# Optimization experiments

Measured on AMD Instinct MI355X. Metric: run time of the kernel, lower is better.

## Reference

```python
import jax, jax.numpy as jnp
import numpy as np

NT, NRV, NR = 100000, 200000, 300000  # tile / road_vertex / road node counts
E = 400000                             # edges per edge type
B, H, P, A = 64, 128, 64, 512          # graphs, hidden, player_state_dim, action_dim


def _gat(h_src, h_dst, src, dst, W, a_s, a_d, b, n_dst):
    # PyG GATConv, heads=1, shared lin for src/dst, no self loops (bipartite)
    hs = h_src @ W                      # [Ns, H]
    hd = h_dst @ W                      # [Nd, H]
    e = jax.nn.leaky_relu((hs @ a_s)[src] + (hd @ a_d)[dst], 0.2)  # [E]
    m = jax.ops.segment_max(e, dst, num_segments=n_dst)
    w = jnp.exp(e - m[dst])
    denom = jax.ops.segment_sum(w, dst, num_segments=n_dst)
    alpha = w / jnp.maximum(denom[dst], 1e-16)                      # segment softmax
    out = jax.ops.segment_sum(alpha[:, None] * hs[src], dst, num_segments=n_dst)
    return out + b


def _mean_pool(x, batch, nb):
    s = jax.ops.segment_sum(x, batch, num_segments=nb)
    c = jax.ops.segment_sum(jnp.ones((x.shape[0],), x.dtype), batch, num_segments=nb)
    return s / jnp.maximum(c, 1.0)[:, None]


def setup_inputs():
    ks = iter(jax.random.split(jax.random.key(0), 64))
    f32 = jnp.float32

    def lin(i, o):
        return (jax.random.normal(next(ks), (i, o), f32) / np.float32(np.sqrt(i)))

    d = {}
    d['x_tile'] = jax.random.normal(next(ks), (NT, 8), f32)
    d['x_rv'] = jax.random.normal(next(ks), (NRV, 13), f32)
    d['x_road'] = jax.random.normal(next(ks), (NR, 4), f32)
    d['x_player'] = jax.random.normal(next(ks), (B, P), f32)
    # node encoders
    d['enc_t_W'] = lin(8, H);  d['enc_t_b'] = jnp.zeros((H,), f32)
    d['enc_rv_W'] = lin(13, H); d['enc_rv_b'] = jnp.zeros((H,), f32)
    d['enc_r_W'] = lin(4, H);  d['enc_r_b'] = jnp.zeros((H,), f32)
    # six GAT convs
    for name in ['rv2t', 't2rv', 'r2rv', 'rv2r', 't2r', 'r2t']:
        d[name + '_W'] = lin(H, H)
        d[name + '_as'] = jax.random.normal(next(ks), (H,), f32) * 0.1
        d[name + '_ad'] = jax.random.normal(next(ks), (H,), f32) * 0.1
        d[name + '_b'] = jnp.zeros((H,), f32)
    # player MLP + output head (input: 3H pooled + H player)
    d['fc1_W'] = lin(P, H); d['fc1_b'] = jnp.zeros((H,), f32)
    d['fc2_W'] = lin(H, H); d['fc2_b'] = jnp.zeros((H,), f32)
    d['out_W'] = lin(4 * H, A); d['out_b'] = jnp.zeros((A,), f32)
    # edges (src bounded by source-type count, dst by dest-type count)
    ri = lambda n, hi: jax.random.randint(n, (E,), 0, hi, jnp.int32)
    d['e_rv2t_src'] = ri(next(ks), NRV); d['e_rv2t_dst'] = ri(next(ks), NT)
    d['e_t2rv_src'] = ri(next(ks), NT);  d['e_t2rv_dst'] = ri(next(ks), NRV)
    d['e_r2rv_src'] = ri(next(ks), NR);  d['e_r2rv_dst'] = ri(next(ks), NRV)
    d['e_rv2r_src'] = ri(next(ks), NRV); d['e_rv2r_dst'] = ri(next(ks), NR)
    d['e_t2r_src'] = ri(next(ks), NT);   d['e_t2r_dst'] = ri(next(ks), NR)
    d['e_r2t_src'] = ri(next(ks), NR);   d['e_r2t_dst'] = ri(next(ks), NT)
    # batch assignment per node type
    d['batch_tile'] = jnp.sort(jax.random.randint(next(ks), (NT,), 0, B, jnp.int32))
    d['batch_rv'] = jnp.sort(jax.random.randint(next(ks), (NRV,), 0, B, jnp.int32))
    d['batch_road'] = jnp.sort(jax.random.randint(next(ks), (NR,), 0, B, jnp.int32))
    return d


def reference(x_tile, x_rv, x_road, x_player,
              enc_t_W, enc_t_b, enc_rv_W, enc_rv_b, enc_r_W, enc_r_b,
              rv2t_W, rv2t_as, rv2t_ad, rv2t_b,
              t2rv_W, t2rv_as, t2rv_ad, t2rv_b,
              r2rv_W, r2rv_as, r2rv_ad, r2rv_b,
              rv2r_W, rv2r_as, rv2r_ad, rv2r_b,
              t2r_W, t2r_as, t2r_ad, t2r_b,
              r2t_W, r2t_as, r2t_ad, r2t_b,
              fc1_W, fc1_b, fc2_W, fc2_b, out_W, out_b,
              e_rv2t_src, e_rv2t_dst, e_t2rv_src, e_t2rv_dst,
              e_r2rv_src, e_r2rv_dst, e_rv2r_src, e_rv2r_dst,
              e_t2r_src, e_t2r_dst, e_r2t_src, e_r2t_dst,
              batch_tile, batch_rv, batch_road):
    # node encoders
    h_t = x_tile @ enc_t_W + enc_t_b
    h_rv = x_rv @ enc_rv_W + enc_rv_b
    h_r = x_road @ enc_r_W + enc_r_b
    # hetero GAT, aggr='sum' over edge types per destination node type
    o_t = (_gat(h_rv, h_t, e_rv2t_src, e_rv2t_dst, rv2t_W, rv2t_as, rv2t_ad, rv2t_b, NT)
           + _gat(h_r, h_t, e_r2t_src, e_r2t_dst, r2t_W, r2t_as, r2t_ad, r2t_b, NT))
    o_rv = (_gat(h_t, h_rv, e_t2rv_src, e_t2rv_dst, t2rv_W, t2rv_as, t2rv_ad, t2rv_b, NRV)
            + _gat(h_r, h_rv, e_r2rv_src, e_r2rv_dst, r2rv_W, r2rv_as, r2rv_ad, r2rv_b, NRV))
    o_r = (_gat(h_rv, h_r, e_rv2r_src, e_rv2r_dst, rv2r_W, rv2r_as, rv2r_ad, rv2r_b, NR)
           + _gat(h_t, h_r, e_t2r_src, e_t2r_dst, t2r_W, t2r_as, t2r_ad, t2r_b, NR))
    # global mean pool per node type, concat -> [B, 3H]
    x_all = jnp.concatenate([_mean_pool(o_t, batch_tile, B),
                             _mean_pool(o_rv, batch_rv, B),
                             _mean_pool(o_r, batch_road, B)], axis=1)
    # player branch
    p = jax.nn.relu(x_player @ fc1_W + fc1_b)
    p = jax.nn.relu(p @ fc2_W + fc2_b)
    x = jnp.concatenate([x_all, p], axis=1)  # [B, 4H]
    return x @ out_W + out_b                 # [B, A]
```

## Files before the change

kernel.cpp:

```cpp
#include <hip/hip_runtime.h>


constexpr int kNT = 100000, kNRV = 200000, kNR = 300000, kE = 400000;
constexpr int kEh   = kE / 2;
constexpr int kTOTE = 6 * kE;
constexpr int kSLOT = 1088;
constexpr int kPSZ  = 6 * kSLOT;
constexpr int kNB   = 256;

struct alignas(8) DRec { _Float16 ld; unsigned short batch; float denom; };

typedef _Float16 h2v __attribute__((ext_vector_type(2)));

constexpr long long OFF_C    = 0;
constexpr long long OFF_VS   = 13056;
constexpr long long OFF_VD   = 13176;
constexpr long long OFF_P    = 13296;
constexpr long long OFF_P8   = 19824;
constexpr long long OFF_XCAT = 72048;
constexpr long long OFF_LS16 = 104816;
constexpr long long OFF_W16  = 704816;
constexpr long long OFF_DREC = 1904816;
constexpr long long OFF_XR   = 4304816;
constexpr long long OFF_PB   = 6904816;

__constant__ const int kLSB[6]  = {0, 200000, 300000, 600000, 800000, 900000};
__constant__ const int kDRB[6]  = {0, 100000, 300000, 500000, 800000, 1100000};
__constant__ const int kDLEN[6] = {100000, 200000, 200000, 300000, 300000, 100000};

__global__ __launch_bounds__(256) void precompute_kernel(
    const float* encW_t, const float* encb_t,
    const float* encW_rv, const float* encb_rv,
    const float* encW_r, const float* encb_r,
    const float* W0, const float* as0, const float* ad0,
    const float* W1, const float* as1, const float* ad1,
    const float* W2, const float* as2, const float* ad2,
    const float* W3, const float* as3, const float* ad3,
    const float* W4, const float* as4, const float* ad4,
    const float* W5, const float* as5, const float* ad5,
    float* Cws, float* vsw, float* vdw)
{
  const float* encW[3] = {encW_t, encW_rv, encW_r};
  const float* encb[3] = {encb_t, encb_rv, encb_r};
  const int    Ks[3]   = {8, 13, 4};
  const float* Wv[6]  = {W0, W1, W2, W3, W4, W5};
  const float* asv[6] = {as0, as1, as2, as3, as4, as5};
  const float* adv[6] = {ad0, ad1, ad2, ad3, ad4, ad5};
  const int srcT[6] = {1, 0, 2, 1, 0, 2};
  const int dstT[6] = {0, 1, 1, 2, 2, 0};

  int et = blockIdx.x >> 2;
  int jc = blockIdx.x & 3;
  int tid = threadIdx.x;
  int st = srcT[et], dt = dstT[et];
  const float* eW = encW[st];
  const float* eB = encb[st];
  int K = Ks[st];
  const float* W = Wv[et];

  float* Cslot = Cws + et * 2176;
  for (int idx = tid; idx < (K + 1) * 32; idx += 256) {
    int r = idx >> 5, jj = idx & 31;
    int j = jc * 32 + jj;
    const float* row = (r < K) ? (eW + r * 128) : eB;
    float acc = 0.f;
    for (int m = 0; m < 128; ++m) acc += row[m] * W[m * 128 + j];
    Cslot[(r < K) ? (r * 128 + j) : (2048 + j)] = acc;
  }

  if (jc == 0) {
    __shared__ float us[128], wvs[128];
    const float* a_s = asv[et];
    const float* a_d = adv[et];
    if (tid < 128) {
      float acc = 0.f;
      for (int j = 0; j < 128; ++j) acc += W[tid * 128 + j] * a_s[j];
      us[tid] = acc;
    } else {
      int m = tid - 128;
      float acc = 0.f;
      for (int j = 0; j < 128; ++j) acc += W[m * 128 + j] * a_d[j];
      wvs[m] = acc;
    }
    __syncthreads();
    if (tid <= K) {
      const float* row = (tid < K) ? (eW + tid * 128) : eB;
      float acc = 0.f;
      for (int m = 0; m < 128; ++m) acc += row[m] * us[m];
      vsw[et * 20 + (tid < K ? tid : 16)] = acc;
    }
    int KD = Ks[dt];
    if (tid >= 32 && tid <= 32 + KD) {
      int k = tid - 32;
      const float* row = (k < KD) ? (encW[dt] + k * 128) : encb[dt];
      float acc = 0.f;
      for (int m = 0; m < 128; ++m) acc += row[m] * wvs[m];
      vdw[et * 20 + (k < KD ? k : 16)] = acc;
    }
  }
}

template <int K, int RH>
__device__ __forceinline__ void prep_one(
    const float* __restrict__ xr, unsigned short b,
    const float* __restrict__ vsA, const float* __restrict__ vsB,
    const float* __restrict__ vdA, const float* __restrict__ vdB,
    _Float16* lsA, _Float16* lsB, DRec* drA, DRec* drB, _Float16* xrec)
{
  float a0 = 0.f, a1 = 0.f, a2 = 0.f, a3 = 0.f;
#pragma unroll
  for (int k = 0; k < K; ++k) {
    float xv = xr[k];
    a0 += xv * vsA[k]; a1 += xv * vsB[k];
    a2 += xv * vdA[k]; a3 += xv * vdB[k];
    xrec[k] = (_Float16)xv;
  }
#pragma unroll
  for (int k = K; k < RH; ++k) xrec[k] = (_Float16)0.f;
  *lsA = (_Float16)(a0 + vsA[16]);
  *lsB = (_Float16)(a1 + vsB[16]);
  DRec rA; rA.ld = (_Float16)(a2 + vdA[16]); rA.batch = b; rA.denom = 0.f;
  DRec rB; rB.ld = (_Float16)(a3 + vdB[16]); rB.batch = b; rB.denom = 0.f;
  *drA = rA;
  *drB = rB;
}

__global__ __launch_bounds__(256) void prep_kernel(
    const float* __restrict__ x_t, const float* __restrict__ x_rv,
    const float* __restrict__ x_r,
    const int* __restrict__ bt, const int* __restrict__ brv,
    const int* __restrict__ br,
    const float* __restrict__ vsw, const float* __restrict__ vdw,
    _Float16* __restrict__ LS16, DRec* __restrict__ DRC,
    _Float16* __restrict__ XR)
{
  int n = blockIdx.x * 256 + threadIdx.x;
  if (n >= kNT + kNRV + kNR) return;
  if (n < kNT) {
    prep_one<8, 8>(x_t + n * 8, (unsigned short)bt[n],
                   vsw + 1 * 20, vsw + 4 * 20, vdw + 0 * 20, vdw + 5 * 20,
                   LS16 + 200000 + n, LS16 + 800000 + n,
                   DRC + 0 + n, DRC + 1100000 + n,
                   XR + (long long)n * 8);
  } else if (n < kNT + kNRV) {
    int m = n - kNT;
    prep_one<13, 16>(x_rv + m * 13, (unsigned short)brv[m],
                     vsw + 0 * 20, vsw + 3 * 20, vdw + 1 * 20, vdw + 2 * 20,
                     LS16 + 0 + m, LS16 + 600000 + m,
                     DRC + 100000 + m, DRC + 300000 + m,
                     XR + 800000 + (long long)m * 16);
  } else {
    int m = n - kNT - kNRV;
    prep_one<4, 4>(x_r + m * 4, (unsigned short)br[m],
                   vsw + 2 * 20, vsw + 5 * 20, vdw + 3 * 20, vdw + 4 * 20,
                   LS16 + 300000 + m, LS16 + 900000 + m,
                   DRC + 500000 + m, DRC + 800000 + m,
                   XR + 4000000 + (long long)m * 4);
  }
}

__global__ __launch_bounds__(256) void passA_kernel(
    const int* s0, const int* s1, const int* s2,
    const int* s3, const int* s4, const int* s5,
    const int* d0, const int* d1, const int* d2,
    const int* d3, const int* d4, const int* d5,
    const _Float16* __restrict__ LS16, DRec* __restrict__ DRC,
    _Float16* __restrict__ W16)
{
  int idx = blockIdx.x * 256 + threadIdx.x;
  if (idx >= kTOTE / 2) return;
  int et = idx / kEh;
  int p = idx - et * kEh;
  const int* sp; const int* dp;
  switch (et) {
    case 0: sp = s0; dp = d0; break;
    case 1: sp = s1; dp = d1; break;
    case 2: sp = s2; dp = d2; break;
    case 3: sp = s3; dp = d3; break;
    case 4: sp = s4; dp = d4; break;
    default: sp = s5; dp = d5; break;
  }
  int lsb = kLSB[et], drb = kDRB[et];
  int2 ss = ((const int2*)sp)[p];
  int2 dd = ((const int2*)dp)[p];
  DRec* r0 = &DRC[drb + dd.x];
  DRec* r1 = &DRC[drb + dd.y];
  float t0 = (float)LS16[lsb + ss.x] + (float)r0->ld;
  float t1 = (float)LS16[lsb + ss.y] + (float)r1->ld;
  t0 = t0 > 0.f ? t0 : 0.2f * t0;
  t1 = t1 > 0.f ? t1 : 0.2f * t1;
  _Float16 h0 = (_Float16)__expf(t0);
  _Float16 h1 = (_Float16)__expf(t1);
  h2v hh; hh.x = h0; hh.y = h1;
  ((h2v*)W16)[idx] = hh;
  unsafeAtomicAdd(&r0->denom, (float)h0);
  unsafeAtomicAdd(&r1->denom, (float)h1);
}

template <int RH>
__device__ __forceinline__ void loadX(const _Float16* __restrict__ xp, float* xv) {
  if constexpr (RH == 4) {
    union { uint2 u; _Float16 h[4]; } U;
    U.u = *(const uint2*)xp;
#pragma unroll
    for (int k = 0; k < RH; ++k) xv[k] = (float)U.h[k];
  } else if constexpr (RH == 8) {
    union { uint4 u; _Float16 h[8]; } U;
    U.u = *(const uint4*)xp;
#pragma unroll
    for (int k = 0; k < RH; ++k) xv[k] = (float)U.h[k];
  } else {
    union { uint4 u[2]; _Float16 h[16]; } U;
    U.u[0] = *(const uint4*)xp;
    U.u[1] = *(const uint4*)(xp + 8);
#pragma unroll
    for (int k = 0; k < RH; ++k) xv[k] = (float)U.h[k];
  }
}

template <int K, int RH>
__device__ __forceinline__ void passB_loop(
    const int* __restrict__ sp, const int* __restrict__ dp,
    int drb, int dlen, long long xrb,
    const h2v* __restrict__ W2et, const DRec* __restrict__ DRC,
    const _Float16* __restrict__ XR, float* __restrict__ lp,
    int start, int stride)
{
  for (int p = start; p < kEh; p += stride) {
    int2 ss = ((const int2*)sp)[p];
    int2 dd = ((const int2*)dp)[p];
    h2v ww = W2et[p];
    DRec r0 = DRC[drb + dd.x];
    DRec r1 = DRC[drb + dd.y];
    const _Float16* xp0 = XR + xrb + (long long)ss.x * RH;
    const _Float16* xp1 = XR + xrb + (long long)ss.y * RH;
    float xv0[RH], xv1[RH];
    loadX<RH>(xp0, xv0);
    loadX<RH>(xp1, xv1);
    float a0 = (float)ww.x / fmaxf(r0.denom, 1e-16f);
    float a1 = (float)ww.y / fmaxf(r1.denom, 1e-16f);
    int b0 = r0.batch, b1 = r1.batch;
#pragma unroll
    for (int k = 0; k < K; ++k) {
      atomicAdd(lp + k * 64 + b0, a0 * xv0[k]);
      atomicAdd(lp + k * 64 + b1, a1 * xv1[k]);
    }
  }
  for (int j = start; j < dlen; j += stride) {
    DRec r = DRC[drb + j];
    if (r.denom > 0.f) atomicAdd(lp + 1024 + r.batch, 1.f);
  }
}

__global__ __launch_bounds__(256) void passB_kernel(
    const int* s0, const int* s1, const int* s2,
    const int* s3, const int* s4, const int* s5,
    const int* d0, const int* d1, const int* d2,
    const int* d3, const int* d4, const int* d5,
    const _Float16* __restrict__ W16, const DRec* __restrict__ DRC,
    const _Float16* __restrict__ XR, float* __restrict__ PB)
{
  __shared__ float lp[kSLOT];
  for (int j = threadIdx.x; j < kSLOT; j += 256) lp[j] = 0.f;
  __syncthreads();
  int et  = blockIdx.x / kNB;
  int blk = blockIdx.x - et * kNB;
  int start = blk * 256 + threadIdx.x;
  int stride = kNB * 256;
  int drb = kDRB[et], dlen = kDLEN[et];
  const h2v* W2et = (const h2v*)(W16 + (long long)et * kE);
  switch (et) {
    case 0: passB_loop<13,16>(s0, d0, drb, dlen, 800000,  W2et, DRC, XR, lp, start, stride); break;
    case 1: passB_loop< 8, 8>(s1, d1, drb, dlen, 0,       W2et, DRC, XR, lp, start, stride); break;
    case 2: passB_loop< 4, 4>(s2, d2, drb, dlen, 4000000, W2et, DRC, XR, lp, start, stride); break;
    case 3: passB_loop<13,16>(s3, d3, drb, dlen, 800000,  W2et, DRC, XR, lp, start, stride); break;
    case 4: passB_loop< 8, 8>(s4, d4, drb, dlen, 0,       W2et, DRC, XR, lp, start, stride); break;
    default: passB_loop<4, 4>(s5, d5, drb, dlen, 4000000, W2et, DRC, XR, lp, start, stride); break;
  }
  __syncthreads();
  float* dst = PB + (long long)blockIdx.x * kSLOT;
  for (int j = threadIdx.x; j < kSLOT; j += 256) dst[j] = lp[j];
}

__global__ __launch_bounds__(256) void reduce1_kernel(
    const float* __restrict__ PB, float* __restrict__ P8)
{
  int jb = blockIdx.x % 26;
  int c  = blockIdx.x / 26;
  int j = jb * 256 + threadIdx.x;
  if (j >= kPSZ) return;
  int et = j / kSLOT;
  int jj = j - et * kSLOT;
  const float* base = PB + ((long long)(et * kNB + c * 32)) * kSLOT + jj;
  float s = 0.f;
#pragma unroll 8
  for (int t = 0; t < 32; ++t) s += base[(long long)t * kSLOT];
  P8[c * kPSZ + j] = s;
}

__global__ __launch_bounds__(256) void reduce2_kernel(
    const float* __restrict__ P8, float* __restrict__ P)
{
  int j = blockIdx.x * 256 + threadIdx.x;
  if (j >= kPSZ) return;
  float s = 0.f;
#pragma unroll
  for (int c = 0; c < 8; ++c) s += P8[c * kPSZ + j];
  P[j] = s;
}

__device__ __forceinline__ int lowb(const int* a, int n, int v) {
  int lo = 0, hi = n;
  while (lo < hi) { int mid = (lo + hi) >> 1; if (a[mid] < v) lo = mid + 1; else hi = mid; }
  return lo;
}

__global__ __launch_bounds__(128) void finalize_kernel(
    const int* __restrict__ bt, const int* __restrict__ brv, const int* __restrict__ br,
    const float* __restrict__ xp,
    const float* __restrict__ fc1W, const float* __restrict__ fc1b,
    const float* __restrict__ fc2W, const float* __restrict__ fc2b,
    const float* __restrict__ b_rv2t, const float* __restrict__ b_r2t,
    const float* __restrict__ b_t2rv, const float* __restrict__ b_r2rv,
    const float* __restrict__ b_rv2r, const float* __restrict__ b_t2r,
    const float* __restrict__ Cws, const float* __restrict__ P,
    float* __restrict__ xcat)
{
  int b = blockIdx.x, tid = threadIdx.x;
  __shared__ float xps[64];
  __shared__ float p1s[128];
  __shared__ int cnts[3];
  if (tid < 64) xps[tid] = xp[b * 64 + tid];
  if (tid < 3) {
    const int* ba = (tid == 0) ? bt : (tid == 1 ? brv : br);
    int N = (tid == 0) ? kNT : (tid == 1 ? kNRV : kNR);
    cnts[tid] = lowb(ba, N, b + 1) - lowb(ba, N, b);
  }
  __syncthreads();
  float a = fc1b[tid];
  for (int k = 0; k < 64; ++k) a += xps[k] * fc1W[k * 128 + tid];
  p1s[tid] = fmaxf(a, 0.f);
  __syncthreads();
  float a2 = fc2b[tid];
  for (int k = 0; k < 128; ++k) a2 += p1s[k] * fc2W[k * 128 + tid];
  xcat[b * 512 + 384 + tid] = fmaxf(a2, 0.f);
  const int etA[3] = {0, 1, 3}, etB[3] = {5, 2, 4};
  const int KAv[3] = {13, 8, 13}, KBv[3] = {4, 4, 8};
  for (int t3 = 0; t3 < 3; ++t3) {
    int eA = etA[t3], eB = etB[t3];
    const float* CA = Cws + eA * 2176;
    const float* CB = Cws + eB * 2176;
    const float* pA = P + eA * kSLOT;
    const float* pB = P + eB * kSLOT;
    float cA = pA[1024 + b];
    float cB = pB[1024 + b];
    float v = cA * CA[2048 + tid] + cB * CB[2048 + tid];
    for (int k = 0; k < KAv[t3]; ++k) v += pA[k * 64 + b] * CA[k * 128 + tid];
    for (int k = 0; k < KBv[t3]; ++k) v += pB[k * 64 + b] * CB[k * 128 + tid];
    float cnt = (float)max(cnts[t3], 1);
    const float* bb1 = (t3 == 0) ? b_rv2t : (t3 == 1 ? b_t2rv : b_rv2r);
    const float* bb2 = (t3 == 0) ? b_r2t  : (t3 == 1 ? b_r2rv : b_t2r);
    xcat[b * 512 + t3 * 128 + tid] = v / cnt + bb1[tid] + bb2[tid];
  }
}

__global__ __launch_bounds__(256) void out_kernel(
    const float* __restrict__ xcat, const float* __restrict__ outW,
    const float* __restrict__ outb, float* __restrict__ out)
{
  int g = blockIdx.x * 256 + threadIdx.x;
  int r = g >> 9, c = g & 511;
  const float* xr = xcat + r * 512;
  float acc = outb[c];
  for (int k = 0; k < 512; ++k) acc += xr[k] * outW[k * 512 + c];
  out[g] = acc;
}

extern "C" void kernel_launch(void* const* d_in, const int* in_sizes, int n_in,
                              void* d_out, int out_size, void* d_ws, size_t ws_size,
                              hipStream_t stream) {
  const float* x_tile   = (const float*)d_in[0];
  const float* x_rv     = (const float*)d_in[1];
  const float* x_road   = (const float*)d_in[2];
  const float* x_player = (const float*)d_in[3];
  const float* enc_t_W  = (const float*)d_in[4];
  const float* enc_t_b  = (const float*)d_in[5];
  const float* enc_rv_W = (const float*)d_in[6];
  const float* enc_rv_b = (const float*)d_in[7];
  const float* enc_r_W  = (const float*)d_in[8];
  const float* enc_r_b  = (const float*)d_in[9];
  const float* W[6]; const float* As[6]; const float* Ad[6]; const float* Bb[6];
  for (int et = 0; et < 6; ++et) {
    W[et]  = (const float*)d_in[10 + 4 * et];
    As[et] = (const float*)d_in[11 + 4 * et];
    Ad[et] = (const float*)d_in[12 + 4 * et];
    Bb[et] = (const float*)d_in[13 + 4 * et];
  }
  const float* fc1W = (const float*)d_in[34];
  const float* fc1b = (const float*)d_in[35];
  const float* fc2W = (const float*)d_in[36];
  const float* fc2b = (const float*)d_in[37];
  const float* outW = (const float*)d_in[38];
  const float* outb = (const float*)d_in[39];
  const int* esrc[6]; const int* edst[6];
  for (int et = 0; et < 6; ++et) {
    esrc[et] = (const int*)d_in[40 + 2 * et];
    edst[et] = (const int*)d_in[41 + 2 * et];
  }
  const int* batch_t  = (const int*)d_in[52];
  const int* batch_rv = (const int*)d_in[53];
  const int* batch_r  = (const int*)d_in[54];

  float* wsF = (float*)d_ws;
  float* Cws  = wsF + OFF_C;
  float* vsw  = wsF + OFF_VS;
  float* vdw  = wsF + OFF_VD;
  float* P    = wsF + OFF_P;
  float* P8   = wsF + OFF_P8;
  float* xcat = wsF + OFF_XCAT;
  _Float16* LS16 = (_Float16*)(wsF + OFF_LS16);
  _Float16* W16  = (_Float16*)(wsF + OFF_W16);
  DRec* DRC  = (DRec*)(wsF + OFF_DREC);
  _Float16* XR = (_Float16*)(wsF + OFF_XR);
  float* PB   = wsF + OFF_PB;
  float* out  = (float*)d_out;

  precompute_kernel<<<24, 256, 0, stream>>>(
      enc_t_W, enc_t_b, enc_rv_W, enc_rv_b, enc_r_W, enc_r_b,
      W[0], As[0], Ad[0], W[1], As[1], Ad[1], W[2], As[2], Ad[2],
      W[3], As[3], Ad[3], W[4], As[4], Ad[4], W[5], As[5], Ad[5],
      Cws, vsw, vdw);

  prep_kernel<<<(kNT + kNRV + kNR + 255) / 256, 256, 0, stream>>>(
      x_tile, x_rv, x_road, batch_t, batch_rv, batch_r, vsw, vdw,
      LS16, DRC, XR);

  passA_kernel<<<(kTOTE / 2 + 255) / 256, 256, 0, stream>>>(
      esrc[0], esrc[1], esrc[2], esrc[3], esrc[4], esrc[5],
      edst[0], edst[1], edst[2], edst[3], edst[4], edst[5],
      LS16, DRC, W16);

  passB_kernel<<<6 * kNB, 256, 0, stream>>>(
      esrc[0], esrc[1], esrc[2], esrc[3], esrc[4], esrc[5],
      edst[0], edst[1], edst[2], edst[3], edst[4], edst[5],
      W16, DRC, XR, PB);

  reduce1_kernel<<<26 * 8, 256, 0, stream>>>(PB, P8);
  reduce2_kernel<<<26, 256, 0, stream>>>(P8, P);

  finalize_kernel<<<64, 128, 0, stream>>>(
      batch_t, batch_rv, batch_r, x_player,
      fc1W, fc1b, fc2W, fc2b,
      Bb[0], Bb[5], Bb[1], Bb[2], Bb[3], Bb[4],
      Cws, P, xcat);

  out_kernel<<<128, 256, 0, stream>>>(xcat, outW, outb, out);

  (void)in_sizes; (void)n_in; (void)out_size; (void)ws_size;
}
```

Before: 571.0 us.

## Split DRec into separate arrays, derive batch ids via boundary search, rebalance passB slots

The interleaved destination record (logit, batch id, denominator) is split into separate half-precision logit and float denominator arrays. Per-node batch ids are no longer stored; graph boundaries are computed once with binary search and a shared-memory lookup resolves each destination's graph. Edge passes now process four edges per thread with int4 loads. PassB is reorganized into 8 slots that split the two large source types by source-index range to balance work, which replaces the two-stage reduction with a single reduce. The costs are an extra six-step search per edge and a redundant full scan of the edge lists in the split slots.

```diff
diff --git a/kernel.cpp b/kernel.cpp
--- a/kernel.cpp
+++ b/kernel.cpp
@@ -2,31 +2,40 @@
 
 
 constexpr int kNT = 100000, kNRV = 200000, kNR = 300000, kE = 400000;
-constexpr int kEh   = kE / 2;
-constexpr int kTOTE = 6 * kE;
+constexpr int kEq   = kE / 4;
 constexpr int kSLOT = 1088;
-constexpr int kPSZ  = 6 * kSLOT;
-constexpr int kNB   = 256;
-
-struct alignas(8) DRec { _Float16 ld; unsigned short batch; float denom; };
+constexpr int kNBB  = 1024;
 
 typedef _Float16 h2v __attribute__((ext_vector_type(2)));
 
 constexpr long long OFF_C    = 0;
 constexpr long long OFF_VS   = 13056;
 constexpr long long OFF_VD   = 13176;
-constexpr long long OFF_P    = 13296;
-constexpr long long OFF_P8   = 19824;
-constexpr long long OFF_XCAT = 72048;
-constexpr long long OFF_LS16 = 104816;
-constexpr long long OFF_W16  = 704816;
-constexpr long long OFF_DREC = 1904816;
-constexpr long long OFF_XR   = 4304816;
-constexpr long long OFF_PB   = 6904816;
+constexpr long long OFF_BD   = 13296;
+constexpr long long OFF_PS   = 13512;
+constexpr long long OFF_XCAT = 22216;
+constexpr long long OFF_LS16 = 54984;
+constexpr long long OFF_LD16 = 654984;
+constexpr long long OFF_PB   = 54984;
+constexpr long long OFF_W16  = 1254984;
+constexpr long long OFF_DN   = 2454984;
+constexpr long long OFF_XR   = 3654984;
 
 __constant__ const int kLSB[6]  = {0, 200000, 300000, 600000, 800000, 900000};
 __constant__ const int kDRB[6]  = {0, 100000, 300000, 500000, 800000, 1100000};
 __constant__ const int kDLEN[6] = {100000, 200000, 200000, 300000, 300000, 100000};
+__constant__ const int kDstT[6] = {0, 1, 1, 2, 2, 0};
+__constant__ const int cSlotEt[8]  = {1, 2, 4, 5, 0, 0, 3, 3};
+__constant__ const int cSlotLo[8]  = {0, 0, 0, 0, 0, 100000, 0, 100000};
+__constant__ const int cSlotHi[8]  = {1 << 30, 1 << 30, 1 << 30, 1 << 30,
+                                      100000, 200000, 100000, 200000};
+__constant__ const int cSlotCnt[8] = {1, 1, 1, 1, 1, 0, 1, 0};
+
+__device__ __forceinline__ int lowb(const int* a, int n, int v) {
+  int lo = 0, hi = n;
+  while (lo < hi) { int mid = (lo + hi) >> 1; if (a[mid] < v) lo = mid + 1; else hi = mid; }
+  return lo;
+}
 
 __global__ __launch_bounds__(256) void precompute_kernel(
     const float* encW_t, const float* encb_t,
@@ -38,8 +47,19 @@
     const float* W3, const float* as3, const float* ad3,
     const float* W4, const float* as4, const float* ad4,
     const float* W5, const float* as5, const float* ad5,
-    float* Cws, float* vsw, float* vdw)
-{
+    const int* bt, const int* brv, const int* br,
+    float* Cws, float* vsw, float* vdw, int* BD)
+{
+  int tid = threadIdx.x;
+  if (blockIdx.x == 24) {
+    if (tid < 3 * 65) {
+      int tt = tid / 65, q = tid - tt * 65;
+      const int* ba = (tt == 0) ? bt : (tt == 1 ? brv : br);
+      int N = (tt == 0) ? kNT : (tt == 1 ? kNRV : kNR);
+      BD[tt * 72 + q] = lowb(ba, N, q);
+    }
+    return;
+  }
   const float* encW[3] = {encW_t, encW_rv, encW_r};
   const float* encb[3] = {encb_t, encb_rv, encb_r};
   const int    Ks[3]   = {8, 13, 4};
@@ -51,7 +71,6 @@
 
   int et = blockIdx.x >> 2;
   int jc = blockIdx.x & 3;
-  int tid = threadIdx.x;
   int st = srcT[et], dt = dstT[et];
   const float* eW = encW[st];
   const float* eB = encb[st];
@@ -102,10 +121,11 @@
 
 template <int K, int RH>
 __device__ __forceinline__ void prep_one(
-    const float* __restrict__ xr, unsigned short b,
+    const float* __restrict__ xr,
     const float* __restrict__ vsA, const float* __restrict__ vsB,
     const float* __restrict__ vdA, const float* __restrict__ vdB,
-    _Float16* lsA, _Float16* lsB, DRec* drA, DRec* drB, _Float16* xrec)
+    _Float16* lsA, _Float16* lsB, _Float16* ldA, _Float16* ldB,
+    float* dnA, float* dnB, _Float16* xrec)
 {
   float a0 = 0.f, a1 = 0.f, a2 = 0.f, a3 = 0.f;
 #pragma unroll
@@ -119,42 +139,43 @@
   for (int k = K; k < RH; ++k) xrec[k] = (_Float16)0.f;
   *lsA = (_Float16)(a0 + vsA[16]);
   *lsB = (_Float16)(a1 + vsB[16]);
-  DRec rA; rA.ld = (_Float16)(a2 + vdA[16]); rA.batch = b; rA.denom = 0.f;
-  DRec rB; rB.ld = (_Float16)(a3 + vdB[16]); rB.batch = b; rB.denom = 0.f;
-  *drA = rA;
-  *drB = rB;
+  *ldA = (_Float16)(a2 + vdA[16]);
+  *ldB = (_Float16)(a3 + vdB[16]);
+  *dnA = 0.f;
+  *dnB = 0.f;
 }
 
 __global__ __launch_bounds__(256) void prep_kernel(
     const float* __restrict__ x_t, const float* __restrict__ x_rv,
     const float* __restrict__ x_r,
-    const int* __restrict__ bt, const int* __restrict__ brv,
-    const int* __restrict__ br,
     const float* __restrict__ vsw, const float* __restrict__ vdw,
-    _Float16* __restrict__ LS16, DRec* __restrict__ DRC,
-    _Float16* __restrict__ XR)
+    _Float16* __restrict__ LS16, _Float16* __restrict__ LD16,
+    float* __restrict__ DN, _Float16* __restrict__ XR)
 {
   int n = blockIdx.x * 256 + threadIdx.x;
   if (n >= kNT + kNRV + kNR) return;
   if (n < kNT) {
-    prep_one<8, 8>(x_t + n * 8, (unsigned short)bt[n],
+    prep_one<8, 8>(x_t + n * 8,
                    vsw + 1 * 20, vsw + 4 * 20, vdw + 0 * 20, vdw + 5 * 20,
                    LS16 + 200000 + n, LS16 + 800000 + n,
-                   DRC + 0 + n, DRC + 1100000 + n,
+                   LD16 + 0 + n, LD16 + 1100000 + n,
+                   DN + 0 + n, DN + 1100000 + n,
                    XR + (long long)n * 8);
   } else if (n < kNT + kNRV) {
     int m = n - kNT;
-    prep_one<13, 16>(x_rv + m * 13, (unsigned short)brv[m],
+    prep_one<13, 16>(x_rv + m * 13,
                      vsw + 0 * 20, vsw + 3 * 20, vdw + 1 * 20, vdw + 2 * 20,
                      LS16 + 0 + m, LS16 + 600000 + m,
-                     DRC + 100000 + m, DRC + 300000 + m,
+                     LD16 + 100000 + m, LD16 + 300000 + m,
+                     DN + 100000 + m, DN + 300000 + m,
                      XR + 800000 + (long long)m * 16);
   } else {
     int m = n - kNT - kNRV;
-    prep_one<4, 4>(x_r + m * 4, (unsigned short)br[m],
+    prep_one<4, 4>(x_r + m * 4,
                    vsw + 2 * 20, vsw + 5 * 20, vdw + 3 * 20, vdw + 4 * 20,
                    LS16 + 300000 + m, LS16 + 900000 + m,
-                   DRC + 500000 + m, DRC + 800000 + m,
+                   LD16 + 500000 + m, LD16 + 800000 + m,
+                   DN + 500000 + m, DN + 800000 + m,
                    XR + 4000000 + (long long)m * 4);
   }
 }
@@ -164,13 +185,13 @@
     const int* s3, const int* s4, const int* s5,
     const int* d0, const int* d1, const int* d2,
     const int* d3, const int* d4, const int* d5,
-    const _Float16* __restrict__ LS16, DRec* __restrict__ DRC,
-    _Float16* __restrict__ W16)
+    const _Float16* __restrict__ LS16, const _Float16* __restrict__ LD16,
+    float* __restrict__ DN, _Float16* __restrict__ W16)
 {
   int idx = blockIdx.x * 256 + threadIdx.x;
-  if (idx >= kTOTE / 2) return;
-  int et = idx / kEh;
-  int p = idx - et * kEh;
+  if (idx >= 6 * kEq) return;
+  int et = idx / kEq;
+  int q = idx - et * kEq;
   const int* sp; const int* dp;
   switch (et) {
     case 0: sp = s0; dp = d0; break;
@@ -181,20 +202,23 @@
     default: sp = s5; dp = d5; break;
   }
   int lsb = kLSB[et], drb = kDRB[et];
-  int2 ss = ((const int2*)sp)[p];
-  int2 dd = ((const int2*)dp)[p];
-  DRec* r0 = &DRC[drb + dd.x];
-  DRec* r1 = &DRC[drb + dd.y];
-  float t0 = (float)LS16[lsb + ss.x] + (float)r0->ld;
-  float t1 = (float)LS16[lsb + ss.y] + (float)r1->ld;
-  t0 = t0 > 0.f ? t0 : 0.2f * t0;
-  t1 = t1 > 0.f ? t1 : 0.2f * t1;
-  _Float16 h0 = (_Float16)__expf(t0);
-  _Float16 h1 = (_Float16)__expf(t1);
-  h2v hh; hh.x = h0; hh.y = h1;
-  ((h2v*)W16)[idx] = hh;
-  unsafeAtomicAdd(&r0->denom, (float)h0);
-  unsafeAtomicAdd(&r1->denom, (float)h1);
+  int4 ss = ((const int4*)sp)[q];
+  int4 dd = ((const int4*)dp)[q];
+  int sa[4] = {ss.x, ss.y, ss.z, ss.w};
+  int da[4] = {dd.x, dd.y, dd.z, dd.w};
+  union { float2 f; _Float16 h[4]; } WU;
+  float wa[4];
+#pragma unroll
+  for (int i = 0; i < 4; ++i) {
+    float t = (float)LS16[lsb + sa[i]] + (float)LD16[drb + da[i]];
+    t = t > 0.f ? t : 0.2f * t;
+    _Float16 h = (_Float16)__expf(t);
+    WU.h[i] = h;
+    wa[i] = (float)h;
+  }
+  ((float2*)(W16 + (long long)et * kE))[q] = WU.f;
+#pragma unroll
+  for (int i = 0; i < 4; ++i) unsafeAtomicAdd(&DN[drb + da[i]], wa[i]);
 }
 
 template <int RH>
@@ -221,34 +245,36 @@
 template <int K, int RH>
 __device__ __forceinline__ void passB_loop(
     const int* __restrict__ sp, const int* __restrict__ dp,
-    int drb, int dlen, long long xrb,
-    const h2v* __restrict__ W2et, const DRec* __restrict__ DRC,
-    const _Float16* __restrict__ XR, float* __restrict__ lp,
-    int start, int stride)
-{
-  for (int p = start; p < kEh; p += stride) {
-    int2 ss = ((const int2*)sp)[p];
-    int2 dd = ((const int2*)dp)[p];
-    h2v ww = W2et[p];
-    DRec r0 = DRC[drb + dd.x];
-    DRec r1 = DRC[drb + dd.y];
-    const _Float16* xp0 = XR + xrb + (long long)ss.x * RH;
-    const _Float16* xp1 = XR + xrb + (long long)ss.y * RH;
-    float xv0[RH], xv1[RH];
-    loadX<RH>(xp0, xv0);
-    loadX<RH>(xp1, xv1);
-    float a0 = (float)ww.x / fmaxf(r0.denom, 1e-16f);
-    float a1 = (float)ww.y / fmaxf(r1.denom, 1e-16f);
-    int b0 = r0.batch, b1 = r1.batch;
-#pragma unroll
-    for (int k = 0; k < K; ++k) {
-      atomicAdd(lp + k * 64 + b0, a0 * xv0[k]);
-      atomicAdd(lp + k * 64 + b1, a1 * xv1[k]);
-    }
-  }
-  for (int j = start; j < dlen; j += stride) {
-    DRec r = DRC[drb + j];
-    if (r.denom > 0.f) atomicAdd(lp + 1024 + r.batch, 1.f);
+    const _Float16* __restrict__ Wet, const float* __restrict__ DN, int drb,
+    const _Float16* __restrict__ XR, long long xrb,
+    const int* __restrict__ bd, float* __restrict__ lp,
+    int lo, int hi, int start, int stride)
+{
+  for (int q = start; q < kEq; q += stride) {
+    int4 ss = ((const int4*)sp)[q];
+    int4 dd = ((const int4*)dp)[q];
+    union { float2 f; _Float16 h[4]; } WU;
+    WU.f = ((const float2*)Wet)[q];
+    int sa[4] = {ss.x, ss.y, ss.z, ss.w};
+    int da[4] = {dd.x, dd.y, dd.z, dd.w};
+#pragma unroll
+    for (int i = 0; i < 4; ++i) {
+      int s = sa[i], d = da[i];
+      if (s >= lo && s < hi) {
+        float dn = DN[drb + d];
+        float alpha = (float)WU.h[i] / fmaxf(dn, 1e-16f);
+        int b = 0;
+#pragma unroll
+        for (int stp = 32; stp >= 1; stp >>= 1) {
+          int nb = b + stp;
+          if (nb <= 63 && bd[nb] <= d) b = nb;
+        }
+        float xv[RH];
+        loadX<RH>(XR + xrb + (long long)s * RH, xv);
+#pragma unroll
+        for (int k = 0; k < K; ++k) atomicAdd(lp + k * 64 + b, alpha * xv[k]);
+      }
+    }
   }
 }
 
@@ -257,85 +283,80 @@
     const int* s3, const int* s4, const int* s5,
     const int* d0, const int* d1, const int* d2,
     const int* d3, const int* d4, const int* d5,
-    const _Float16* __restrict__ W16, const DRec* __restrict__ DRC,
-    const _Float16* __restrict__ XR, float* __restrict__ PB)
+    const _Float16* __restrict__ W16, const float* __restrict__ DN,
+    const _Float16* __restrict__ XR, const int* __restrict__ BDg,
+    float* __restrict__ PB)
 {
   __shared__ float lp[kSLOT];
-  for (int j = threadIdx.x; j < kSLOT; j += 256) lp[j] = 0.f;
+  __shared__ int bd[65];
+  int tid = threadIdx.x;
+  for (int j = tid; j < kSLOT; j += 256) lp[j] = 0.f;
+  int slot = blockIdx.x & 7;
+  int blk = blockIdx.x >> 3;
+  int et = cSlotEt[slot];
+  if (tid < 65) bd[tid] = BDg[kDstT[et] * 72 + tid];
   __syncthreads();
-  int et  = blockIdx.x / kNB;
-  int blk = blockIdx.x - et * kNB;
-  int start = blk * 256 + threadIdx.x;
-  int stride = kNB * 256;
-  int drb = kDRB[et], dlen = kDLEN[et];
-  const h2v* W2et = (const h2v*)(W16 + (long long)et * kE);
+  int lo = cSlotLo[slot], hi = cSlotHi[slot];
+  int start = blk * 256 + tid;
+  int stride = 128 * 256;
+  int drb = kDRB[et];
+  const _Float16* Wet = W16 + (long long)et * kE;
   switch (et) {
-    case 0: passB_loop<13,16>(s0, d0, drb, dlen, 800000,  W2et, DRC, XR, lp, start, stride); break;
-    case 1: passB_loop< 8, 8>(s1, d1, drb, dlen, 0,       W2et, DRC, XR, lp, start, stride); break;
-    case 2: passB_loop< 4, 4>(s2, d2, drb, dlen, 4000000, W2et, DRC, XR, lp, start, stride); break;
-    case 3: passB_loop<13,16>(s3, d3, drb, dlen, 800000,  W2et, DRC, XR, lp, start, stride); break;
-    case 4: passB_loop< 8, 8>(s4, d4, drb, dlen, 0,       W2et, DRC, XR, lp, start, stride); break;
-    default: passB_loop<4, 4>(s5, d5, drb, dlen, 4000000, W2et, DRC, XR, lp, start, stride); break;
+    case 0: passB_loop<13, 16>(s0, d0, Wet, DN, drb, XR, 800000,  bd, lp, lo, hi, start, stride); break;
+    case 1: passB_loop< 8,  8>(s1, d1, Wet, DN, drb, XR, 0,       bd, lp, lo, hi, start, stride); break;
+    case 2: passB_loop< 4,  4>(s2, d2, Wet, DN, drb, XR, 4000000, bd, lp, lo, hi, start, stride); break;
+    case 3: passB_loop<13, 16>(s3, d3, Wet, DN, drb, XR, 800000,  bd, lp, lo, hi, start, stride); break;
+    case 4: passB_loop< 8,  8>(s4, d4, Wet, DN, drb, XR, 0,       bd, lp, lo, hi, start, stride); break;
+    default: passB_loop<4,  4>(s5, d5, Wet, DN, drb, XR, 4000000, bd, lp, lo, hi, start, stride); break;
+  }
+  if (cSlotCnt[slot]) {
+    int dlen = kDLEN[et];
+    for (int j = start; j < dlen; j += stride) {
+      if (DN[drb + j] > 0.f) {
+        int b = 0;
+#pragma unroll
+        for (int stp = 32; stp >= 1; stp >>= 1) {
+          int nb = b + stp;
+          if (nb <= 63 && bd[nb] <= j) b = nb;
+        }
+        atomicAdd(lp + 1024 + b, 1.f);
+      }
+    }
   }
   __syncthreads();
   float* dst = PB + (long long)blockIdx.x * kSLOT;
-  for (int j = threadIdx.x; j < kSLOT; j += 256) dst[j] = lp[j];
+  for (int j = tid; j < kSLOT; j += 256) dst[j] = lp[j];
 }
 
 __global__ __launch_bounds__(256) void reduce1_kernel(
-    const float* __restrict__ PB, float* __restrict__ P8)
-{
-  int jb = blockIdx.x % 26;
-  int c  = blockIdx.x / 26;
+    const float* __restrict__ PB, float* __restrict__ PS)
+{
+  int slot = blockIdx.x / 5;
+  int jb = blockIdx.x - slot * 5;
   int j = jb * 256 + threadIdx.x;
-  if (j >= kPSZ) return;
-  int et = j / kSLOT;
-  int jj = j - et * kSLOT;
-  const float* base = PB + ((long long)(et * kNB + c * 32)) * kSLOT + jj;
+  if (j >= kSLOT) return;
   float s = 0.f;
 #pragma unroll 8
-  for (int t = 0; t < 32; ++t) s += base[(long long)t * kSLOT];
-  P8[c * kPSZ + j] = s;
-}
-
-__global__ __launch_bounds__(256) void reduce2_kernel(
-    const float* __restrict__ P8, float* __restrict__ P)
-{
-  int j = blockIdx.x * 256 + threadIdx.x;
-  if (j >= kPSZ) return;
-  float s = 0.f;
-#pragma unroll
-  for (int c = 0; c < 8; ++c) s += P8[c * kPSZ + j];
-  P[j] = s;
-}
-
-__device__ __forceinline__ int lowb(const int* a, int n, int v) {
-  int lo = 0, hi = n;
-  while (lo < hi) { int mid = (lo + hi) >> 1; if (a[mid] < v) lo = mid + 1; else hi = mid; }
-  return lo;
+  for (int blk = 0; blk < 128; ++blk)
+    s += PB[(long long)(blk * 8 + slot) * kSLOT + j];
+  PS[slot * kSLOT + j] = s;
 }
 
 __global__ __launch_bounds__(128) void finalize_kernel(
-    const int* __restrict__ bt, const int* __restrict__ brv, const int* __restrict__ br,
+    const int* __restrict__ BDg,
     const float* __restrict__ xp,
     const float* __restrict__ fc1W, const float* __restrict__ fc1b,
     const float* __restrict__ fc2W, const float* __restrict__ fc2b,
     const float* __restrict__ b_rv2t, const float* __restrict__ b_r2t,
     const float* __restrict__ b_t2rv, const float* __restrict__ b_r2rv,
     const float* __restrict__ b_rv2r, const float* __restrict__ b_t2r,
-    const float* __restrict__ Cws, const float* __restrict__ P,
+    const float* __restrict__ Cws, const float* __restrict__ PS,
     float* __restrict__ xcat)
 {
   int b = blockIdx.x, tid = threadIdx.x;
   __shared__ float xps[64];
   __shared__ float p1s[128];
-  __shared__ int cnts[3];
   if (tid < 64) xps[tid] = xp[b * 64 + tid];
-  if (tid < 3) {
-    const int* ba = (tid == 0) ? bt : (tid == 1 ? brv : br);
-    int N = (tid == 0) ? kNT : (tid == 1 ? kNRV : kNR);
-    cnts[tid] = lowb(ba, N, b + 1) - lowb(ba, N, b);
-  }
   __syncthreads();
   float a = fc1b[tid];
   for (int k = 0; k < 64; ++k) a += xps[k] * fc1W[k * 128 + tid];
@@ -344,23 +365,37 @@
   float a2 = fc2b[tid];
   for (int k = 0; k < 128; ++k) a2 += p1s[k] * fc2W[k * 128 + tid];
   xcat[b * 512 + 384 + tid] = fmaxf(a2, 0.f);
+
   const int etA[3] = {0, 1, 3}, etB[3] = {5, 2, 4};
   const int KAv[3] = {13, 8, 13}, KBv[3] = {4, 4, 8};
+  const int slotA[6] = {4, 0, 1, 6, 2, 3};
+  const int slotB[6] = {5, -1, -1, 7, -1, -1};
   for (int t3 = 0; t3 < 3; ++t3) {
     int eA = etA[t3], eB = etB[t3];
     const float* CA = Cws + eA * 2176;
     const float* CB = Cws + eB * 2176;
-    const float* pA = P + eA * kSLOT;
-    const float* pB = P + eB * kSLOT;
-    float cA = pA[1024 + b];
-    float cB = pB[1024 + b];
+    int sA1 = slotA[eA], sA2 = slotB[eA];
+    int sB1 = slotA[eB], sB2 = slotB[eB];
+    const float* PA1 = PS + sA1 * kSLOT;
+    const float* PA2 = (sA2 >= 0) ? (PS + sA2 * kSLOT) : nullptr;
+    const float* PB1 = PS + sB1 * kSLOT;
+    const float* PB2 = (sB2 >= 0) ? (PS + sB2 * kSLOT) : nullptr;
+    float cA = PA1[1024 + b] + (PA2 ? PA2[1024 + b] : 0.f);
+    float cB = PB1[1024 + b] + (PB2 ? PB2[1024 + b] : 0.f);
     float v = cA * CA[2048 + tid] + cB * CB[2048 + tid];
-    for (int k = 0; k < KAv[t3]; ++k) v += pA[k * 64 + b] * CA[k * 128 + tid];
-    for (int k = 0; k < KBv[t3]; ++k) v += pB[k * 64 + b] * CB[k * 128 + tid];
-    float cnt = (float)max(cnts[t3], 1);
+    for (int k = 0; k < KAv[t3]; ++k) {
+      float pv = PA1[k * 64 + b] + (PA2 ? PA2[k * 64 + b] : 0.f);
+      v += pv * CA[k * 128 + tid];
+    }
+    for (int k = 0; k < KBv[t3]; ++k) {
+      float pv = PB1[k * 64 + b] + (PB2 ? PB2[k * 64 + b] : 0.f);
+      v += pv * CB[k * 128 + tid];
+    }
+    int cnt = BDg[t3 * 72 + b + 1] - BDg[t3 * 72 + b];
+    float cntf = (float)max(cnt, 1);
     const float* bb1 = (t3 == 0) ? b_rv2t : (t3 == 1 ? b_t2rv : b_rv2r);
     const float* bb2 = (t3 == 0) ? b_r2t  : (t3 == 1 ? b_r2rv : b_t2r);
-    xcat[b * 512 + t3 * 128 + tid] = v / cnt + bb1[tid] + bb2[tid];
+    xcat[b * 512 + t3 * 128 + tid] = v / cntf + bb1[tid] + bb2[tid];
   }
 }
 
@@ -415,44 +450,44 @@
   float* Cws  = wsF + OFF_C;
   float* vsw  = wsF + OFF_VS;
   float* vdw  = wsF + OFF_VD;
-  float* P    = wsF + OFF_P;
-  float* P8   = wsF + OFF_P8;
+  int*   BD   = (int*)(wsF + OFF_BD);
+  float* PS   = wsF + OFF_PS;
   float* xcat = wsF + OFF_XCAT;
   _Float16* LS16 = (_Float16*)(wsF + OFF_LS16);
-  _Float16* W16  = (_Float16*)(wsF + OFF_W16);
-  DRec* DRC  = (DRec*)(wsF + OFF_DREC);
+  _Float16* LD16 = (_Float16*)(wsF + OFF_LD16);
+  float* PB   = wsF + OFF_PB;
+  _Float16* W16 = (_Float16*)(wsF + OFF_W16);
+  float* DN   = wsF + OFF_DN;
   _Float16* XR = (_Float16*)(wsF + OFF_XR);
-  float* PB   = wsF + OFF_PB;
   float* out  = (float*)d_out;
 
-  precompute_kernel<<<24, 256, 0, stream>>>(
+  precompute_kernel<<<25, 256, 0, stream>>>(
       enc_t_W, enc_t_b, enc_rv_W, enc_rv_b, enc_r_W, enc_r_b,
       W[0], As[0], Ad[0], W[1], As[1], Ad[1], W[2], As[2], Ad[2],
       W[3], As[3], Ad[3], W[4], As[4], Ad[4], W[5], As[5], Ad[5],
-      Cws, vsw, vdw);
+      batch_t, batch_rv, batch_r,
+      Cws, vsw, vdw, BD);
 
   prep_kernel<<<(kNT + kNRV + kNR + 255) / 256, 256, 0, stream>>>(
-      x_tile, x_rv, x_road, batch_t, batch_rv, batch_r, vsw, vdw,
-      LS16, DRC, XR);
-
-  passA_kernel<<<(kTOTE / 2 + 255) / 256, 256, 0, stream>>>(
+      x_tile, x_rv, x_road, vsw, vdw, LS16, LD16, DN, XR);
+
+  passA_kernel<<<(6 * kEq + 255) / 256, 256, 0, stream>>>(
       esrc[0], esrc[1], esrc[2], esrc[3], esrc[4], esrc[5],
       edst[0], edst[1], edst[2], edst[3], edst[4], edst[5],
-      LS16, DRC, W16);
-
-  passB_kernel<<<6 * kNB, 256, 0, stream>>>(
+      LS16, LD16, DN, W16);
+
+  passB_kernel<<<kNBB, 256, 0, stream>>>(
       esrc[0], esrc[1], esrc[2], esrc[3], esrc[4], esrc[5],
       edst[0], edst[1], edst[2], edst[3], edst[4], edst[5],
-      W16, DRC, XR, PB);
-
-  reduce1_kernel<<<26 * 8, 256, 0, stream>>>(PB, P8);
-  reduce2_kernel<<<26, 256, 0, stream>>>(P8, P);
+      W16, DN, XR, BD, PB);
+
+  reduce1_kernel<<<40, 256, 0, stream>>>(PB, PS);
 
   finalize_kernel<<<64, 128, 0, stream>>>(
-      batch_t, batch_rv, batch_r, x_player,
+      BD, x_player,
       fc1W, fc1b, fc2W, fc2b,
       Bb[0], Bb[5], Bb[1], Bb[2], Bb[3], Bb[4],
-      Cws, P, xcat);
+      Cws, PS, xcat);
 
   out_kernel<<<128, 256, 0, stream>>>(xcat, outW, outb, out);
 
```

Result: faster. 554.1 us (-3.0%).
